# Kernel tuning notes

Measured on AMD Instinct MI355X. Metric: run time of the kernel, lower is better.

Reference implementation:

```python
import jax, jax.numpy as jnp
import numpy as np

N_SAMPLES = 131072
N_FEATURES = 512
N_KERNELS = 29


def setup_inputs() -> dict:
    key = jax.random.key(0)
    k1, k2, k3 = jax.random.split(key, 3)
    Xs = jax.random.normal(k1, (N_SAMPLES, N_FEATURES), dtype=jnp.float32)
    Xt = jax.random.normal(k2, (N_SAMPLES, N_FEATURES), dtype=jnp.float32)
    # unit-sum random betas, as in the torch default constructor
    r = jax.random.uniform(k3, (N_KERNELS, 1), dtype=jnp.float32)
    betas = r / jnp.sum(r)
    return {"Xs": Xs, "Xt": Xt, "betas": betas}


def reference(Xs, Xt, betas):
    # default length-scales: gammas = 2 ** arange(-3.5, 3.75, 0.25) -> 29 kernels
    gammas = jnp.power(jnp.float32(2.0), jnp.arange(-3.5, 3.75, 0.25, dtype=jnp.float32))  # [29]

    n, f = Xs.shape
    m = (n // 2) * 2  # drop last sample if odd
    X = Xs[:m].reshape(m // 2, 2, f)  # pairs (x_{2i-1}, x_{2i})
    Y = Xt[:m].reshape(m // 2, 2, f)  # pairs (y_{2i-1}, y_{2i})

    def sq_dist(a, b):  # [P, F] -> [P]
        d = a - b
        return jnp.sum(d * d, axis=1)

    # quadruple v_i = [x, x', y, y']; distances (x,x'), (y,y'), (x,y'), (x',y)
    D = jnp.stack(
        [
            sq_dist(X[:, 0], X[:, 1]),
            sq_dist(Y[:, 0], Y[:, 1]),
            sq_dist(X[:, 0], Y[:, 1]),
            sq_dist(X[:, 1], Y[:, 0]),
        ],
        axis=1,
    )  # [P, 4]

    # K[g, p, c] = exp(-D[p, c] / (2 * gamma_g^2)) -- all 29 kernels in one broadcast
    inv_two_gamma_sq = 1.0 / (2.0 * gammas * gammas)  # [29]
    K = jnp.exp(-D[None, :, :] * inv_two_gamma_sq[:, None, None])  # [29, P, 4]

    h_u = K[..., 0] + K[..., 1] - K[..., 2] - K[..., 3]  # [29, P]
    hat_d = jnp.mean(h_u, axis=1, keepdims=True)  # [29, 1]
    return (betas.T @ hat_d).squeeze(0)  # shape (1,)
```

## Files before the change

kernel.cpp:

```cpp
#include <hip/hip_runtime.h>

#define N_SAMPLES 131072
#define N_FEAT    512
#define N_PAIRS   (N_SAMPLES / 2)
#define N_KER     29
#define MAX_NB    1024

struct Batch {
  float4 x0, x1, xp0, xp1, y0, y1, yp0, yp1;
};

__device__ __forceinline__ void load_batch(const float* __restrict__ Xs,
                                           const float* __restrict__ Xt,
                                           int p, int o0, Batch& b) {
  const float* x = Xs + (size_t)p * (size_t)(2 * N_FEAT);
  const float* y = Xt + (size_t)p * (size_t)(2 * N_FEAT);
  b.x0  = *reinterpret_cast<const float4*>(x + o0);
  b.x1  = *reinterpret_cast<const float4*>(x + o0 + 256);
  b.xp0 = *reinterpret_cast<const float4*>(x + o0 + N_FEAT);
  b.xp1 = *reinterpret_cast<const float4*>(x + o0 + N_FEAT + 256);
  b.y0  = *reinterpret_cast<const float4*>(y + o0);
  b.y1  = *reinterpret_cast<const float4*>(y + o0 + 256);
  b.yp0 = *reinterpret_cast<const float4*>(y + o0 + N_FEAT);
  b.yp1 = *reinterpret_cast<const float4*>(y + o0 + N_FEAT + 256);
}

__device__ __forceinline__ void compute_pair(const Batch& b, double c, int lane,
                                             double& acc) {
  double d0 = 0.0, d1 = 0.0, d2 = 0.0, d3 = 0.0;

#define MMD_ACC(A, AP, B, BP)                                   \
  {                                                             \
    const double ax  = (double)(A);                             \
    const double axp = (double)(AP);                            \
    const double ay  = (double)(B);                             \
    const double ayp = (double)(BP);                            \
    double t;                                                   \
    t = ax - axp; d0 = fma(t, t, d0);                           \
    t = ay - ayp; d1 = fma(t, t, d1);                           \
    t = ax - ayp; d2 = fma(t, t, d2);                           \
    t = axp - ay; d3 = fma(t, t, d3);                           \
  }
  MMD_ACC(b.x0.x, b.xp0.x, b.y0.x, b.yp0.x)
  MMD_ACC(b.x0.y, b.xp0.y, b.y0.y, b.yp0.y)
  MMD_ACC(b.x0.z, b.xp0.z, b.y0.z, b.yp0.z)
  MMD_ACC(b.x0.w, b.xp0.w, b.y0.w, b.yp0.w)
  MMD_ACC(b.x1.x, b.xp1.x, b.y1.x, b.yp1.x)
  MMD_ACC(b.x1.y, b.xp1.y, b.y1.y, b.yp1.y)
  MMD_ACC(b.x1.z, b.xp1.z, b.y1.z, b.yp1.z)
  MMD_ACC(b.x1.w, b.xp1.w, b.y1.w, b.yp1.w)
#undef MMD_ACC

#pragma unroll
  for (int s = 32; s > 0; s >>= 1) {
    d0 += __shfl_xor(d0, s);
    d1 += __shfl_xor(d1, s);
    d2 += __shfl_xor(d2, s);
    d3 += __shfl_xor(d3, s);
  }

  if (lane < N_KER) {
    acc += exp(-d0 * c) + exp(-d1 * c) - exp(-d2 * c) - exp(-d3 * c);
  }
}

__global__ __launch_bounds__(256) void mmd_partial(
    const float* __restrict__ Xs, const float* __restrict__ Xt,
    double* __restrict__ ws, int nwaves) {
  const int tid   = threadIdx.x;
  const int lane  = tid & 63;
  const int wib   = tid >> 6;
  const int gwave = blockIdx.x * 4 + wib;
  const int o0    = lane * 4;

  const double c = exp2(6.0 - 0.5 * (double)lane);
  double acc = 0.0;

  int p = gwave;
  if (p < N_PAIRS) {
    Batch A, B;
    load_batch(Xs, Xt, p, o0, A);
    int pn = p + nwaves;
    bool pendingA = true;
    while (pn < N_PAIRS) {
      load_batch(Xs, Xt, pn, o0, B);
      compute_pair(A, c, lane, acc);
      pn += nwaves;
      if (pn < N_PAIRS) {
        load_batch(Xs, Xt, pn, o0, A);
        compute_pair(B, c, lane, acc);
        pn += nwaves;
      } else {
        compute_pair(B, c, lane, acc);
        pendingA = false;
        break;
      }
    }
    if (pendingA) compute_pair(A, c, lane, acc);
  }

  __shared__ double sacc[4][32];
  if (lane < 32) sacc[wib][lane] = (lane < N_KER) ? acc : 0.0;
  __syncthreads();
  if (tid < 32) {
    const double s = sacc[0][tid] + sacc[1][tid] + sacc[2][tid] + sacc[3][tid];
    ws[(size_t)blockIdx.x * 32 + tid] = s;
  }
}

__global__ __launch_bounds__(1024) void mmd_final(
    const double* __restrict__ ws, const float* __restrict__ betas,
    float* __restrict__ out, int nb) {
  const int tid = threadIdx.x;
  double acc = 0.0;
  const int total = nb * 32;
  for (int i = tid; i < total; i += 1024) {
    const int g = i & 31;
    if (g < N_KER) acc += (double)betas[g] * ws[i];
  }
  __shared__ double s[1024];
  s[tid] = acc;
  __syncthreads();
  for (int ofs = 512; ofs > 0; ofs >>= 1) {
    if (tid < ofs) s[tid] += s[tid + ofs];
    __syncthreads();
  }
  if (tid == 0) out[0] = (float)(s[0] / (double)N_PAIRS);
}

extern "C" void kernel_launch(void* const* d_in, const int* in_sizes, int n_in,
                              void* d_out, int out_size, void* d_ws, size_t ws_size,
                              hipStream_t stream) {
  const float* Xs    = (const float*)d_in[0];
  const float* Xt    = (const float*)d_in[1];
  const float* betas = (const float*)d_in[2];
  float*  out = (float*)d_out;
  double* ws  = (double*)d_ws;

  int nb = (int)(ws_size / (32 * sizeof(double)));
  if (nb > MAX_NB) nb = MAX_NB;
  if (nb < 1) nb = 1;

  mmd_partial<<<nb, 256, 0, stream>>>(Xs, Xt, ws, nb * 4);
  mmd_final<<<1, 1024, 0, stream>>>(ws, betas, out, nb);
}
```

Before: 108.2 us.

## Give each wave a contiguous pair chunk with four-deep load pipelining

Replaces the strided grid loop with a contiguous chunk of pairs per wave and keeps four batches in flight, loading the next batch right after computing each one. Adds a launch-bounds occupancy hint, uses readfirstlane for the wave index, and rounds the block count down to a power of two so the chunk divides evenly. The goal is to keep more memory requests outstanding and hide latency on this bandwidth-bound reduction. In exchange it uses more registers, and it assumes cpw is at least 4 and divisible by 4, which only holds for power-of-two block counts.

```diff
diff --git a/kernel.cpp b/kernel.cpp
--- a/kernel.cpp
+++ b/kernel.cpp
@@ -5,6 +5,7 @@
 #define N_PAIRS   (N_SAMPLES / 2)
 #define N_KER     29
 #define MAX_NB    1024
+#define PAIR_F    (2 * N_FEAT)
 
 struct Batch {
   float4 x0, x1, xp0, xp1, y0, y1, yp0, yp1;
@@ -13,8 +14,8 @@
 __device__ __forceinline__ void load_batch(const float* __restrict__ Xs,
                                            const float* __restrict__ Xt,
                                            int p, int o0, Batch& b) {
-  const float* x = Xs + (size_t)p * (size_t)(2 * N_FEAT);
-  const float* y = Xt + (size_t)p * (size_t)(2 * N_FEAT);
+  const float* x = Xs + (size_t)p * PAIR_F;
+  const float* y = Xt + (size_t)p * PAIR_F;
   b.x0  = *reinterpret_cast<const float4*>(x + o0);
   b.x1  = *reinterpret_cast<const float4*>(x + o0 + 256);
   b.xp0 = *reinterpret_cast<const float4*>(x + o0 + N_FEAT);
@@ -64,40 +65,38 @@
   }
 }
 
-__global__ __launch_bounds__(256) void mmd_partial(
+__global__ __launch_bounds__(256, 3) void mmd_partial(
     const float* __restrict__ Xs, const float* __restrict__ Xt,
     double* __restrict__ ws, int nwaves) {
-  const int tid   = threadIdx.x;
-  const int lane  = tid & 63;
-  const int wib   = tid >> 6;
-  const int gwave = blockIdx.x * 4 + wib;
-  const int o0    = lane * 4;
+  const int tid  = threadIdx.x;
+  const int lane = tid & 63;
+  const int wib  = tid >> 6;
+  const int gw   = __builtin_amdgcn_readfirstlane(blockIdx.x * 4 + wib);
+  const int cpw  = N_PAIRS / nwaves;
+  const int o0   = lane * 4;
 
   const double c = exp2(6.0 - 0.5 * (double)lane);
   double acc = 0.0;
 
-  int p = gwave;
-  if (p < N_PAIRS) {
-    Batch A, B;
-    load_batch(Xs, Xt, p, o0, A);
-    int pn = p + nwaves;
-    bool pendingA = true;
-    while (pn < N_PAIRS) {
-      load_batch(Xs, Xt, pn, o0, B);
-      compute_pair(A, c, lane, acc);
-      pn += nwaves;
-      if (pn < N_PAIRS) {
-        load_batch(Xs, Xt, pn, o0, A);
-        compute_pair(B, c, lane, acc);
-        pn += nwaves;
-      } else {
-        compute_pair(B, c, lane, acc);
-        pendingA = false;
-        break;
-      }
-    }
-    if (pendingA) compute_pair(A, c, lane, acc);
+  const int p0 = gw * cpw;
+  Batch A, B, C, D;
+  load_batch(Xs, Xt, p0 + 0, o0, A);
+  load_batch(Xs, Xt, p0 + 1, o0, B);
+  load_batch(Xs, Xt, p0 + 2, o0, C);
+  load_batch(Xs, Xt, p0 + 3, o0, D);
+
+  int p = p0 + 4;
+  for (int rep = 0; rep < cpw / 4 - 1; ++rep) {
+    compute_pair(A, c, lane, acc); load_batch(Xs, Xt, p + 0, o0, A);
+    compute_pair(B, c, lane, acc); load_batch(Xs, Xt, p + 1, o0, B);
+    compute_pair(C, c, lane, acc); load_batch(Xs, Xt, p + 2, o0, C);
+    compute_pair(D, c, lane, acc); load_batch(Xs, Xt, p + 3, o0, D);
+    p += 4;
   }
+  compute_pair(A, c, lane, acc);
+  compute_pair(B, c, lane, acc);
+  compute_pair(C, c, lane, acc);
+  compute_pair(D, c, lane, acc);
 
   __shared__ double sacc[4][32];
   if (lane < 32) sacc[wib][lane] = (lane < N_KER) ? acc : 0.0;
@@ -137,9 +136,9 @@
   float*  out = (float*)d_out;
   double* ws  = (double*)d_ws;
 
-  int nb = (int)(ws_size / (32 * sizeof(double)));
-  if (nb > MAX_NB) nb = MAX_NB;
-  if (nb < 1) nb = 1;
+  size_t nb_fit = ws_size / (32 * sizeof(double));
+  int nb = 1;
+  while ((size_t)(nb * 2) <= nb_fit && nb * 2 <= MAX_NB) nb *= 2;
 
   mmd_partial<<<nb, 256, 0, stream>>>(Xs, Xt, ws, nb * 4);
   mmd_final<<<1, 1024, 0, stream>>>(ws, betas, out, nb);
```

Measured after the change: 229.5 us. 2.12x slower.
